# Optimization experiments

Measured on AMD Instinct MI355X. Metric: run time of the kernel, lower is better.

The kernel has to match this reference:

```python
import jax, jax.numpy as jnp
import numpy as np
import math

N_HEADS = 16
ROPE_BASE = 10000.0


def rotate_half(x):
    x1 = x[..., ::2]
    x2 = x[..., 1::2]
    return jnp.stack((-x2, x1), axis=-1).reshape(x.shape)


def rope_tables(seq_len, head_dim, dtype):
    inv_freq = 1.0 / (ROPE_BASE ** (jnp.arange(0, head_dim, 2, dtype=jnp.float32) / head_dim))
    positions = jnp.arange(seq_len, dtype=jnp.float32)
    freqs = jnp.outer(positions, inv_freq)            # [S, hd/2]
    emb = jnp.concatenate((freqs, freqs), axis=-1)    # [S, hd]  (matches torch cat convention)
    cos = jnp.cos(emb)[None, None, :, :].astype(dtype)
    sin = jnp.sin(emb)[None, None, :, :].astype(dtype)
    return cos, sin


def setup_inputs() -> dict:
    key = jax.random.key(0)
    k1, k2, k3 = jax.random.split(key, 3)
    B, S, D = 2, 2048, 1024
    x = jax.random.normal(k1, (B, S, D), dtype=jnp.float32)
    # causal lower-triangular mask, broadcastable over batch and heads
    mask = jnp.tril(jnp.ones((S, S), dtype=jnp.int32))[None, None, :, :]
    w_qkv = jax.random.normal(k2, (D, 3 * D), dtype=jnp.float32) * 0.02
    w_out = jax.random.normal(k3, (D, D), dtype=jnp.float32) * 0.02
    return {"x": x, "mask": mask, "w_qkv": w_qkv, "w_out": w_out}


def reference(x, mask, w_qkv, w_out):
    B, S, D = x.shape
    H = N_HEADS
    hd = D // H
    qkv = (x @ w_qkv).reshape(B, S, 3, H, hd)
    qkv = jnp.transpose(qkv, (2, 0, 3, 1, 4))         # [3, B, H, S, hd]
    q, k, v = qkv[0], qkv[1], qkv[2]
    cos, sin = rope_tables(S, hd, x.dtype)
    q = q * cos + rotate_half(q) * sin
    k = k * cos + rotate_half(k) * sin
    scale = math.sqrt(hd)
    attn = jnp.einsum("bhsd,bhtd->bhst", q, k) / scale
    attn = jnp.where(mask == 0, -jnp.inf, attn)
    attn = jax.nn.softmax(attn, axis=-1)              # dropout p=0.0 -> identity
    out = jnp.einsum("bhst,bhtd->bhsd", attn, v)
    out = jnp.transpose(out, (0, 2, 1, 3)).reshape(B, S, D)
    return out @ w_out
```

## Files before the change

kernel.cpp:

```cpp
#include <hip/hip_runtime.h>
#include <stdint.h>

typedef unsigned short u16;
typedef __bf16 bf16x8 __attribute__((ext_vector_type(8)));
typedef float f32x4 __attribute__((ext_vector_type(4)));

#define S_LEN 2048
#define NH    16
#define DM    1024
#define N3    3072
#define MROWS 4096

__device__ __forceinline__ float b2f(u16 u) {
  unsigned int v = ((unsigned int)u) << 16;
  return __builtin_bit_cast(float, v);
}
__device__ __forceinline__ u16 f2b(float f) {
  unsigned int v = __builtin_bit_cast(unsigned int, f);
  v += 0x7fffu + ((v >> 16) & 1u);
  return (u16)(v >> 16);
}
__device__ __forceinline__ u16 f2b_trunc(float f) {
  return (u16)(__builtin_bit_cast(unsigned int, f) >> 16);
}
__device__ __forceinline__ bf16x8 ld8(const u16* p) { return *(const bf16x8*)p; }
__device__ __forceinline__ f32x4 mfma16(bf16x8 a, bf16x8 b, f32x4 c) {
  return __builtin_amdgcn_mfma_f32_16x16x32_bf16(a, b, c, 0, 0, 0);
}
__device__ __forceinline__ void glds16(const void* g, void* l) {
  __builtin_amdgcn_global_load_lds(
      (const __attribute__((address_space(1))) unsigned int*)g,
      (__attribute__((address_space(3))) unsigned int*)l, 16, 0, 0);
}
__device__ __forceinline__ int bfish(unsigned int w) {
  unsigned int e = (w >> 7) & 0xffu;
  return (e >= 100u && e <= 134u) ? 1 : 0;
}
__device__ __forceinline__ void wave_cnt_add(int* cnt, int s, int lane) {
  s += __shfl_down(s, 32);
  s += __shfl_down(s, 16);
  s += __shfl_down(s, 8);
  s += __shfl_down(s, 4);
  s += __shfl_down(s, 2);
  s += __shfl_down(s, 1);
  if (lane == 0) atomicAdd(cnt, s);
}

__global__ __launch_bounds__(256) void prep_kernel(const void* __restrict__ x,
                                                   const void* __restrict__ wqkv,
                                                   const void* __restrict__ wout,
                                                   u16* __restrict__ xb,
                                                   u16* __restrict__ wqT,
                                                   u16* __restrict__ woT,
                                                   float* __restrict__ cs,
                                                   int* __restrict__ flag) {
  const int bx = blockIdx.x;
  const int t = threadIdx.x;
  if (bx < 2048) {
    __shared__ int cnt;
    if (t == 0) cnt = 0;
    __syncthreads();
    size_t i = (size_t)bx * 256 + t;
    const uint4* xv = (const uint4*)x;
    uint4 probe = xv[i];
    unsigned int wds[4]; *(uint4*)wds = probe;
    wave_cnt_add(&cnt, bfish(wds[0]) + bfish(wds[1]) + bfish(wds[2]) + bfish(wds[3]),
                 t & 63);
    __syncthreads();
    const int isbf = cnt > 512;
    if (t == 0) *flag = isbf;
    if (isbf) {
      ((uint4*)xb)[i] = probe;
    } else {
      const float4* xf4 = (const float4*)x;
      uint2* xb2 = (uint2*)xb;
      #pragma unroll
      for (int half = 0; half < 2; ++half) {
        const size_t idx = (size_t)bx * 512 + half * 256 + t;
        const float4 v = xf4[idx];
        u16 pk[4];
        pk[0] = f2b(v.x); pk[1] = f2b(v.y); pk[2] = f2b(v.z); pk[3] = f2b(v.w);
        xb2[idx] = *(const uint2*)pk;
      }
    }
    return;
  }
  if (bx < 2560) {
    int i = (bx - 2048) * 256 + t;
    int s = i >> 6, d = i & 63;
    int f = d & 31;
    float invf = expf(-(float)(2 * f) * (1.0f / 64.0f) * logf(10000.0f));
    float th = (float)s * invf;
    float sv, cv;
    sincosf(th, &sv, &cv);
    cs[i * 2] = cv; cs[i * 2 + 1] = sv;
    return;
  }
  const int wq = bx < 3328;
  const int id = wq ? (bx - 2560) : (bx - 3328);
  const int ncx = wq ? 48 : 16;
  const void* in = wq ? wqkv : wout;
  u16* out = wq ? wqT : woT;
  const int C = wq ? 3072 : 1024;
  const int c0 = (id % ncx) * 64, r0 = (id / ncx) * 64;
  __shared__ int cnt;
  __shared__ u16 L[4096];
  if (t == 0) cnt = 0;
  __syncthreads();
  const unsigned int* wv = (const unsigned int*)in;
  size_t off = (((size_t)id) * 256 + t) & 262143;
  wave_cnt_add(&cnt, bfish(wv[off]), t & 63);
  __syncthreads();
  const int fl = cnt > 128;
  if (fl) {
    #pragma unroll
    for (int it = 0; it < 2; ++it) {
      int c = it * 256 + t;
      int rl = c >> 3, cseg = c & 7;
      uint4 v = *(const uint4*)((const u16*)in + (size_t)(r0 + rl) * C + c0 + cseg * 8);
      u16 e[8]; *(uint4*)e = v;
      #pragma unroll
      for (int jj = 0; jj < 8; ++jj) {
        int cl = cseg * 8 + jj;
        L[cl * 64 + (rl ^ (cseg << 3))] = e[jj];
      }
    }
  } else {
    const float* inf_ = (const float*)in;
    #pragma unroll
    for (int it = 0; it < 16; ++it) {
      int c = it * 256 + t;
      int rl = c >> 6, cl = c & 63;
      L[cl * 64 + (rl ^ ((cl >> 3) << 3))] = f2b(inf_[(size_t)(r0 + rl) * C + c0 + cl]);
    }
  }
  __syncthreads();
  #pragma unroll
  for (int it = 0; it < 2; ++it) {
    int c = it * 256 + t;
    int cl = c >> 3, rseg = c & 7;
    uint4 v = *(const uint4*)(L + cl * 64 + (((rseg ^ (cl >> 3)) & 7) << 3));
    *(uint4*)(out + (size_t)(c0 + cl) * 1024 + r0 + rseg * 8) = v;
  }
}


#define PHASE_PRE() do { \
  asm volatile("" ::: "memory"); \
  __builtin_amdgcn_s_barrier(); \
  asm volatile("s_waitcnt lgkmcnt(0)" ::: "memory"); \
  __builtin_amdgcn_sched_barrier(0); \
  __builtin_amdgcn_s_setprio(1); \
} while (0)

#define PHASE_POST() do { \
  __builtin_amdgcn_s_setprio(0); \
  asm volatile("" ::: "memory"); \
  __builtin_amdgcn_s_barrier(); \
} while (0)

#define LOADA(P) \
  _Pragma("unroll") \
  for (int ii = 0; ii < 2; ++ii) { \
    const int row = wr * 64 + ((P) * 2 + ii) * 16 + ln; \
    _Pragma("unroll") \
    for (int kk = 0; kk < 2; ++kk) \
      a[ii][kk] = ld8(Ap + row * 64 + (((kk * 4 + quad) ^ (row & 7)) << 3)); \
  }

#define MFMAQ(P) \
  _Pragma("unroll") \
  for (int ii = 0; ii < 2; ++ii) { \
    _Pragma("unroll") \
    for (int j = 0; j < 4; ++j) { \
      acc[(P) * 2 + ii][j] = mfma16(a[ii][0], b[j][0], acc[(P) * 2 + ii][j]); \
      acc[(P) * 2 + ii][j] = mfma16(a[ii][1], b[j][1], acc[(P) * 2 + ii][j]); \
    } \
  }

__global__ __launch_bounds__(256) void gemm_qkv(const u16* __restrict__ A,
                                                const u16* __restrict__ Bt,
                                                u16* __restrict__ Qo,
                                                u16* __restrict__ Ko,
                                                u16* __restrict__ Vt,
                                                const float* __restrict__ cs) {
  __shared__ u16 smem[2][16384];
  const int t = threadIdx.x;
  const int lane = t & 63, wave = t >> 6;
  const int ln = lane & 15, quad = lane >> 4;
  const int wr = wave >> 1, wc = wave & 1;
  const int m0 = blockIdx.x * 128, n0 = blockIdx.y * 128;
  const u16* gA = A + (size_t)m0 * 1024;
  const u16* gB = Bt + (size_t)n0 * 1024;
  f32x4 acc[4][4] = {};

  auto stage_t = [&](u16* lds, const u16* g, int k0) {
    #pragma unroll
    for (int it = 0; it < 4; ++it) {
      const int c = it * 256 + t;
      const int row = c >> 3, sg = (c & 7) ^ (row & 7);
      glds16(g + (size_t)row * 1024 + k0 + sg * 8, (char*)lds + c * 16);
    }
  };

  stage_t(&smem[0][0],    gA, 0);
  stage_t(&smem[0][8192], gB, 0);
  stage_t(&smem[1][8192], gB, 64);
  asm volatile("s_waitcnt vmcnt(4)" ::: "memory");
  __builtin_amdgcn_s_barrier();

  for (int kt = 0; kt < 16; ++kt) {
    const int p = kt & 1;
    u16* Ap = &smem[p][0];
    u16* Bp = &smem[p][8192];
    u16* Aq = &smem[p ^ 1][0];
    const int kA = (kt + 1) * 64, kB = (kt + 2) * 64;
    bf16x8 b[4][2], a[2][2];
    #pragma unroll
    for (int j = 0; j < 4; ++j) {
      const int row = wc * 64 + j * 16 + ln;
      #pragma unroll
      for (int kk = 0; kk < 2; ++kk)
        b[j][kk] = ld8(Bp + row * 64 + (((kk * 4 + quad) ^ (row & 7)) << 3));
    }
    LOADA(0);
    if (kt < 15) stage_t(Aq, gA, kA);
    PHASE_PRE(); MFMAQ(0); PHASE_POST();
    LOADA(1);
    if (kt < 14) stage_t(Bp, gB, kB);
    PHASE_PRE(); MFMAQ(1);
    __builtin_amdgcn_s_setprio(0);
    if (kt < 14) { asm volatile("s_waitcnt vmcnt(4)" ::: "memory"); }
    else         { asm volatile("s_waitcnt vmcnt(0)" ::: "memory"); }
    asm volatile("" ::: "memory");
    __builtin_amdgcn_s_barrier();
  }

  u16* Tl = &smem[0][0];
  const int which = n0 >> 10;
  const int b_ = m0 >> 11;
  const int s0 = m0 & 2047;
  const int h0 = (n0 & 1023) >> 6;

  if (which < 2) {
    const float qs = which ? 1.0f : 0.18033688011112042f;
    const float2* cs2 = (const float2*)cs;
    #pragma unroll
    for (int i = 0; i < 4; ++i) {
      const int slb = wr * 64 + i * 16 + quad * 4;
      #pragma unroll
      for (int j = 0; j < 4; ++j) {
        const int c = wc * 64 + j * 16 + ln;
        const int d = c & 63;
        const float sgn = (d & 1) ? 1.0f : -1.0f;
        #pragma unroll
        for (int r = 0; r < 4; ++r) {
          const int sl = slb + r;
          const float v = acc[i][j][r];
          const float pp = __shfl_xor(v, 1);
          const float2 cv = cs2[(size_t)(s0 + sl) * 64 + d];
          const float val = (v * cv.x + sgn * pp * cv.y) * qs;
          *(u16*)((char*)Tl + sl * 256 + ((((c >> 3) + 2 * (sl & 7)) & 15) << 4)
                  + ((c & 7) << 1)) = f2b(val);
        }
      }
    }
    __syncthreads();
    u16* dst = which ? Ko : Qo;
    #pragma unroll
    for (int it = 0; it < 8; ++it) {
      const int g = it * 256 + t;
      const int ch = g & 15, sl = g >> 4;
      const int h = ch >> 3, c3 = ch & 7;
      const uint4 vv = *(const uint4*)((const char*)Tl + sl * 256
                        + (((ch + 2 * (sl & 7)) & 15) << 4));
      *(uint4*)(dst + ((size_t)(b_ * NH + h0 + h) * S_LEN + s0 + sl) * 64 + c3 * 8) = vv;
    }
  } else {
    #pragma unroll
    for (int i = 0; i < 4; ++i) {
      const int slb = wr * 64 + i * 16 + quad * 4;
      #pragma unroll
      for (int j = 0; j < 4; ++j) {
        const int c = wc * 64 + j * 16 + ln;
        u16 pk[4];
        #pragma unroll
        for (int r = 0; r < 4; ++r) pk[r] = f2b(acc[i][j][r]);
        *(uint2*)((char*)Tl + c * 256 + ((((slb >> 3) + c) & 15) << 4)
                  + ((slb & 7) << 1)) = *(const uint2*)pk;
      }
    }
    __syncthreads();
    #pragma unroll
    for (int it = 0; it < 8; ++it) {
      const int g = it * 256 + t;
      const int sc = g & 15, cd = g >> 4;
      const int h = cd >> 6, d = cd & 63;
      const uint4 vv = *(const uint4*)((const char*)Tl + cd * 256
                        + (((sc + cd) & 15) << 4));
      *(uint4*)(&Vt[((size_t)((b_ * NH + h0 + h) * 64 + d)) * S_LEN + s0 + sc * 8]) = vv;
    }
  }
}

#undef PHASE_PRE
#undef PHASE_POST
#undef LOADA
#undef MFMAQ

__global__ __launch_bounds__(256) void attn_kernel(const u16* __restrict__ Qb,
                                                   const u16* __restrict__ Kb,
                                                   const u16* __restrict__ Vt,
                                                   u16* __restrict__ Ao) {
  __shared__ u16 smem[20480];
  u16* Kl = smem;
  u16* Vl = smem + 8192;
  u16* Pl = smem + 16384;
  const int t = threadIdx.x;
  const int lane = t & 63, w = t >> 6;
  const int ln = lane & 15, quad = lane >> 4;
  const int i = blockIdx.x;
  const int xcd = i & 7;
  const int j = i >> 3;
  const int bh = (xcd << 2) | (j & 3);
  const int q5 = j >> 2;
  const int g = q5 & 7, s5 = q5 >> 3;
  const int qt = (s5 & 1) ? (31 - ((s5 >> 1) << 3) - g) : (((s5 >> 1) << 3) + g);
  const int q0 = qt * 64;
  const int b = bh >> 4, h = bh & 15;
  const u16* Qbh = Qb + (size_t)bh * (S_LEN * 64);
  const u16* Kbh = Kb + (size_t)bh * (S_LEN * 64);
  const u16* Vtbh = Vt + (size_t)bh * (64 * S_LEN);
  u16* Plw = Pl + w * 1024;
  u16* AoBase = Ao + (size_t)b * S_LEN * DM + h * 64;

  auto stage = [&](int kt, int bufi) {
    u16* kd = Kl + bufi * 4096;
    u16* vd = Vl + bufi * 4096;
    const u16* kg = Kbh + (size_t)kt * 64 * 64;
    const u16* vg = Vtbh + (size_t)kt * 64;
    #pragma unroll
    for (int it = 0; it < 2; ++it) {
      int c = it * 256 + t;
      int row = c >> 3, sg = (c & 7) ^ (row & 7);
      glds16((const char*)kg + ((size_t)row * 64 + sg * 8) * 2,   (char*)kd + c * 16);
      glds16((const char*)vg + ((size_t)row * 2048 + sg * 8) * 2, (char*)vd + c * 16);
    }
  };

  bf16x8 bq[2];
  #pragma unroll
  for (int kk = 0; kk < 2; ++kk)
    bq[kk] = ld8(Qbh + (size_t)(q0 + w * 16 + ln) * 64 + kk * 32 + quad * 8);

  f32x4 o[4] = {};
  float l = 0.f;

  stage(0, 0);
  __syncthreads();

  for (int kt = 0; kt <= qt; ++kt) {
    const int bufi = kt & 1;
    if (kt < qt) stage(kt + 1, bufi ^ 1);
    const u16* Kb_ = Kl + bufi * 4096;
    const u16* Vb_ = Vl + bufi * 4096;

    f32x4 st[4] = {};
    #pragma unroll
    for (int kk = 0; kk < 2; ++kk)
      #pragma unroll
      for (int ct = 0; ct < 4; ++ct) {
        bf16x8 ak = ld8(Kb_ + (ct * 16 + ln) * 64 + (((kk * 4 + quad) ^ (ln & 7)) << 3));
        st[ct] = mfma16(ak, bq[kk], st[ct]);
      }

    const bool diag = (kt == qt);
    #pragma unroll
    for (int ct = 0; ct < 4; ++ct) {
      u16 pk[4];
      #pragma unroll
      for (int r = 0; r < 4; ++r) {
        float p;
        if (diag && (ct * 16 + quad * 4 + r) > (w * 16 + ln)) p = 0.f;
        else p = __builtin_amdgcn_exp2f(st[ct][r]);
        l += p;
        pk[r] = f2b_trunc(p);
      }
      *(uint2*)(Plw + ln * 64 + ((((ct * 2) + (quad >> 1)) ^ (ln & 7)) << 3)
                + ((quad & 1) << 2)) = *(const uint2*)pk;
    }

    #pragma unroll
    for (int k4 = 0; k4 < 2; ++k4) {
      bf16x8 bp = ld8(Plw + ln * 64 + (((k4 * 4 + quad) ^ (ln & 7)) << 3));
      #pragma unroll
      for (int dt = 0; dt < 4; ++dt) {
        bf16x8 av = ld8(Vb_ + (dt * 16 + ln) * 64 + (((k4 * 4 + quad) ^ (ln & 7)) << 3));
        o[dt] = mfma16(av, bp, o[dt]);
      }
    }
    __syncthreads();
  }

  l += __shfl_xor(l, 16);
  l += __shfl_xor(l, 32);
  const float inv = 1.f / l;
  const size_t qrow = (size_t)(q0 + w * 16 + ln) * DM;
  #pragma unroll
  for (int dt = 0; dt < 4; ++dt) {
    u16 pk[4];
    #pragma unroll
    for (int r = 0; r < 4; ++r) pk[r] = f2b(o[dt][r] * inv);
    *(uint2*)(AoBase + qrow + dt * 16 + quad * 4) = *(const uint2*)pk;
  }
}

template <int TM>
__global__ __launch_bounds__(256) void gemm_out_t(const u16* __restrict__ A,
                                                  const u16* __restrict__ Bt,
                                                  void* __restrict__ Out,
                                                  const int* __restrict__ flag) {
  constexpr int MI = TM / 32;
  __shared__ u16 smem[(TM + 128) * 64];
  u16* Al = smem;
  u16* Bl = smem + TM * 64;
  const int t = threadIdx.x;
  const int lane = t & 63, wave = t >> 6;
  const int ln = lane & 15, quad = lane >> 4;
  const int wr = wave >> 1, wc = wave & 1;
  const int m0 = blockIdx.x * TM, n0 = blockIdx.y * 128;
  const char* Ab = (const char*)A;
  const char* Bb = (const char*)Bt;
  f32x4 acc[MI][4] = {};

  for (int k0 = 0; k0 < 1024; k0 += 64) {
    __syncthreads();
    #pragma unroll
    for (int it = 0; it < TM / 32; ++it) {
      const int c = it * 256 + t;
      const int row = c >> 3, sg = (c & 7) ^ (row & 7);
      glds16(Ab + ((size_t)(m0 + row) * 1024 + k0 + sg * 8) * 2, (char*)Al + c * 16);
    }
    #pragma unroll
    for (int it = 0; it < 4; ++it) {
      const int c = it * 256 + t;
      const int row = c >> 3, sg = (c & 7) ^ (row & 7);
      glds16(Bb + ((size_t)(n0 + row) * 1024 + k0 + sg * 8) * 2, (char*)Bl + c * 16);
    }
    __syncthreads();
    bf16x8 a[MI][2], b[4][2];
    #pragma unroll
    for (int i = 0; i < MI; ++i) {
      const int row = wr * (TM / 2) + i * 16 + ln;
      #pragma unroll
      for (int kk = 0; kk < 2; ++kk)
        a[i][kk] = ld8(Al + row * 64 + (((kk * 4 + quad) ^ (row & 7)) << 3));
    }
    #pragma unroll
    for (int j = 0; j < 4; ++j) {
      const int row = wc * 64 + j * 16 + ln;
      #pragma unroll
      for (int kk = 0; kk < 2; ++kk)
        b[j][kk] = ld8(Bl + row * 64 + (((kk * 4 + quad) ^ (row & 7)) << 3));
    }
    #pragma unroll
    for (int i = 0; i < MI; ++i)
      #pragma unroll
      for (int j = 0; j < 4; ++j) {
        acc[i][j] = mfma16(a[i][0], b[j][0], acc[i][j]);
        acc[i][j] = mfma16(a[i][1], b[j][1], acc[i][j]);
      }
  }

  const int fl = *flag;
  #pragma unroll
  for (int i = 0; i < MI; ++i)
    #pragma unroll
    for (int j = 0; j < 4; ++j)
      #pragma unroll
      for (int r = 0; r < 4; ++r) {
        int m = m0 + wr * (TM / 2) + i * 16 + quad * 4 + r;
        int c = n0 + wc * 64 + j * 16 + ln;
        float v = acc[i][j][r];
        if (fl) ((u16*)Out)[(size_t)m * DM + c] = f2b(v);
        else    ((float*)Out)[(size_t)m * DM + c] = v;
      }
}

extern "C" void kernel_launch(void* const* d_in, const int* in_sizes, int n_in,
                              void* d_out, int out_size, void* d_ws, size_t ws_size,
                              hipStream_t stream) {
  (void)in_sizes; (void)n_in; (void)out_size; (void)ws_size;
  const void* x    = d_in[0];
  const void* wqkv = d_in[2];
  const void* wout = d_in[3];
  char* ws = (char*)d_ws;
  u16*  xb   = (u16*)(ws + 0);
  u16*  Ao   = xb;
  u16*  wqT  = (u16*)(ws + 8388608);
  u16*  woT  = (u16*)(ws + 14680064);
  u16*  Qb   = (u16*)(ws + 16777216);
  u16*  Kb   = (u16*)(ws + 25165824);
  u16*  Vt   = (u16*)(ws + 33554432);
  float* cs  = (float*)(ws + 41943040);
  int*  flag = (int*)(ws + 42991616);

  prep_kernel<<<3584, 256, 0, stream>>>(x, wqkv, wout, xb, wqT, woT, cs, flag);
  gemm_qkv<<<dim3(32, 24), 256, 0, stream>>>(xb, wqT, Qb, Kb, Vt, cs);
  attn_kernel<<<1024, 256, 0, stream>>>(Qb, Kb, Vt, Ao);
  gemm_out_t<64><<<dim3(64, 8), 256, 0, stream>>>(Ao, woT, d_out, flag);
}
```

Baseline: 174.4 us.

## Software-pipeline output projection GEMM with double-buffered LDS and phased MFMA

```diff
diff --git a/kernel.cpp b/kernel.cpp
--- a/kernel.cpp
+++ b/kernel.cpp
@@ -144,7 +144,6 @@
   }
 }
 
-
 #define PHASE_PRE() do { \
   asm volatile("" ::: "memory"); \
   __builtin_amdgcn_s_barrier(); \
@@ -302,11 +301,6 @@
     }
   }
 }
-
-#undef PHASE_PRE
-#undef PHASE_POST
-#undef LOADA
-#undef MFMAQ
 
 __global__ __launch_bounds__(256) void attn_kernel(const u16* __restrict__ Qb,
                                                    const u16* __restrict__ Kb,
@@ -415,77 +409,110 @@
   }
 }
 
-template <int TM>
-__global__ __launch_bounds__(256) void gemm_out_t(const u16* __restrict__ A,
-                                                  const u16* __restrict__ Bt,
-                                                  void* __restrict__ Out,
-                                                  const int* __restrict__ flag) {
-  constexpr int MI = TM / 32;
-  __shared__ u16 smem[(TM + 128) * 64];
-  u16* Al = smem;
-  u16* Bl = smem + TM * 64;
+__global__ __launch_bounds__(256) void gemm_out(const u16* __restrict__ A,
+                                                const u16* __restrict__ Bt,
+                                                void* __restrict__ Out,
+                                                const int* __restrict__ flag) {
+  __shared__ u16 smem[2][12288];
   const int t = threadIdx.x;
   const int lane = t & 63, wave = t >> 6;
   const int ln = lane & 15, quad = lane >> 4;
   const int wr = wave >> 1, wc = wave & 1;
-  const int m0 = blockIdx.x * TM, n0 = blockIdx.y * 128;
-  const char* Ab = (const char*)A;
-  const char* Bb = (const char*)Bt;
-  f32x4 acc[MI][4] = {};
-
-  for (int k0 = 0; k0 < 1024; k0 += 64) {
-    __syncthreads();
-    #pragma unroll
-    for (int it = 0; it < TM / 32; ++it) {
+  const int m0 = blockIdx.x * 64, n0 = blockIdx.y * 128;
+  const u16* gA = A + (size_t)m0 * 1024;
+  const u16* gB = Bt + (size_t)n0 * 1024;
+  f32x4 acc[2][4] = {};
+
+  auto stage_A = [&](u16* lds, int k0) {
+    #pragma unroll
+    for (int it = 0; it < 2; ++it) {
       const int c = it * 256 + t;
       const int row = c >> 3, sg = (c & 7) ^ (row & 7);
-      glds16(Ab + ((size_t)(m0 + row) * 1024 + k0 + sg * 8) * 2, (char*)Al + c * 16);
-    }
+      glds16(gA + (size_t)row * 1024 + k0 + sg * 8, (char*)lds + c * 16);
+    }
+  };
+  auto stage_B = [&](u16* lds, int k0) {
     #pragma unroll
     for (int it = 0; it < 4; ++it) {
       const int c = it * 256 + t;
       const int row = c >> 3, sg = (c & 7) ^ (row & 7);
-      glds16(Bb + ((size_t)(n0 + row) * 1024 + k0 + sg * 8) * 2, (char*)Bl + c * 16);
-    }
-    __syncthreads();
-    bf16x8 a[MI][2], b[4][2];
-    #pragma unroll
-    for (int i = 0; i < MI; ++i) {
-      const int row = wr * (TM / 2) + i * 16 + ln;
-      #pragma unroll
-      for (int kk = 0; kk < 2; ++kk)
-        a[i][kk] = ld8(Al + row * 64 + (((kk * 4 + quad) ^ (row & 7)) << 3));
-    }
+      glds16(gB + (size_t)row * 1024 + k0 + sg * 8, (char*)lds + c * 16);
+    }
+  };
+
+  stage_A(&smem[0][0], 0);
+  stage_B(&smem[0][4096], 0);
+  stage_B(&smem[1][4096], 64);
+  asm volatile("s_waitcnt vmcnt(4)" ::: "memory");
+  __builtin_amdgcn_s_barrier();
+
+  for (int kt = 0; kt < 16; ++kt) {
+    const int p = kt & 1;
+    u16* Ap = &smem[p][0];
+    u16* Bp = &smem[p][4096];
+    u16* Aq = &smem[p ^ 1][0];
+    const int kA = (kt + 1) * 64, kB = (kt + 2) * 64;
+    bf16x8 b[4][2], a[2][2];
     #pragma unroll
     for (int j = 0; j < 4; ++j) {
       const int row = wc * 64 + j * 16 + ln;
       #pragma unroll
       for (int kk = 0; kk < 2; ++kk)
-        b[j][kk] = ld8(Bl + row * 64 + (((kk * 4 + quad) ^ (row & 7)) << 3));
-    }
-    #pragma unroll
-    for (int i = 0; i < MI; ++i)
-      #pragma unroll
-      for (int j = 0; j < 4; ++j) {
-        acc[i][j] = mfma16(a[i][0], b[j][0], acc[i][j]);
-        acc[i][j] = mfma16(a[i][1], b[j][1], acc[i][j]);
-      }
+        b[j][kk] = ld8(Bp + row * 64 + (((kk * 4 + quad) ^ (row & 7)) << 3));
+    }
+    {
+      const int row = wr * 32 + ln;
+      #pragma unroll
+      for (int kk = 0; kk < 2; ++kk)
+        a[0][kk] = ld8(Ap + row * 64 + (((kk * 4 + quad) ^ (row & 7)) << 3));
+    }
+    if (kt < 15) stage_A(Aq, kA);
+    PHASE_PRE();
+    #pragma unroll
+    for (int j = 0; j < 4; ++j) {
+      acc[0][j] = mfma16(a[0][0], b[j][0], acc[0][j]);
+      acc[0][j] = mfma16(a[0][1], b[j][1], acc[0][j]);
+    }
+    PHASE_POST();
+    {
+      const int row = wr * 32 + 16 + ln;
+      #pragma unroll
+      for (int kk = 0; kk < 2; ++kk)
+        a[1][kk] = ld8(Ap + row * 64 + (((kk * 4 + quad) ^ (row & 7)) << 3));
+    }
+    if (kt < 14) stage_B(Bp, kB);
+    PHASE_PRE();
+    #pragma unroll
+    for (int j = 0; j < 4; ++j) {
+      acc[1][j] = mfma16(a[1][0], b[j][0], acc[1][j]);
+      acc[1][j] = mfma16(a[1][1], b[j][1], acc[1][j]);
+    }
+    __builtin_amdgcn_s_setprio(0);
+    if (kt < 14) { asm volatile("s_waitcnt vmcnt(4)" ::: "memory"); }
+    else         { asm volatile("s_waitcnt vmcnt(0)" ::: "memory"); }
+    asm volatile("" ::: "memory");
+    __builtin_amdgcn_s_barrier();
   }
 
   const int fl = *flag;
   #pragma unroll
-  for (int i = 0; i < MI; ++i)
+  for (int i = 0; i < 2; ++i)
     #pragma unroll
     for (int j = 0; j < 4; ++j)
       #pragma unroll
       for (int r = 0; r < 4; ++r) {
-        int m = m0 + wr * (TM / 2) + i * 16 + quad * 4 + r;
+        int m = m0 + wr * 32 + i * 16 + quad * 4 + r;
         int c = n0 + wc * 64 + j * 16 + ln;
         float v = acc[i][j][r];
         if (fl) ((u16*)Out)[(size_t)m * DM + c] = f2b(v);
         else    ((float*)Out)[(size_t)m * DM + c] = v;
       }
 }
+
+#undef PHASE_PRE
+#undef PHASE_POST
+#undef LOADA
+#undef MFMAQ
 
 extern "C" void kernel_launch(void* const* d_in, const int* in_sizes, int n_in,
                               void* d_out, int out_size, void* d_ws, size_t ws_size,
@@ -508,5 +535,5 @@
   prep_kernel<<<3584, 256, 0, stream>>>(x, wqkv, wout, xb, wqT, woT, cs, flag);
   gemm_qkv<<<dim3(32, 24), 256, 0, stream>>>(xb, wqT, Qb, Kb, Vt, cs);
   attn_kernel<<<1024, 256, 0, stream>>>(Qb, Kb, Vt, Ao);
-  gemm_out_t<64><<<dim3(64, 8), 256, 0, stream>>>(Ao, woT, d_out, flag);
-}
+  gemm_out<<<dim3(64, 8), 256, 0, stream>>>(Ao, woT, d_out, flag);
+}
```

Result: no change. 171.7 us (-1.6%).
